# Kernel optimization log

Measured on AMD Instinct MI355X. Metric: run time of the kernel, lower is better.

The kernel has to match this reference:

```python
import jax, jax.numpy as jnp
import numpy as np

DECAY = 0.99
EPS = 1e-10
COMMIT = 0.25
K = 1024
D = 64


def setup_inputs() -> dict:
    key = jax.random.key(0)
    k1, k2, k3, k4 = jax.random.split(key, 4)
    return {
        "z_e": jax.random.normal(k1, (64, 64, 32, 32), dtype=jnp.float32),
        "embedding_w": jax.random.normal(k2, (K, D), dtype=jnp.float32),
        "ema_cluster_size": jax.random.uniform(k3, (K,), dtype=jnp.float32),
        "ema_w": jax.random.normal(k4, (K, D), dtype=jnp.float32),
    }


def reference(z_e, embedding_w, ema_cluster_size, ema_w):
    # [B, C, H, W] -> [B, H, W, C] -> [N, D]
    z_nhwc = jnp.transpose(z_e, (0, 2, 3, 1))
    z_flat = z_nhwc.reshape(-1, z_nhwc.shape[-1])

    # Squared-euclidean distances via ||z||^2 + ||e||^2 - 2 z e^T  -> [N, K]
    z_sq = jnp.sum(z_flat * z_flat, axis=1, keepdims=True)
    e_sq = jnp.sum(embedding_w * embedding_w, axis=1)
    distances = z_sq + e_sq - 2.0 * (z_flat @ embedding_w.T)

    indices = jnp.argmin(distances, axis=1)                      # [N]
    encodings = jax.nn.one_hot(indices, K, dtype=z_flat.dtype)   # [N, K]

    quantized = embedding_w[indices].reshape(z_nhwc.shape)       # [B, H, W, C]

    # --- EMA codebook update (training path; no-grad in original) ---
    counts = jnp.sum(encodings, axis=0)                          # [K]
    new_cluster_size = DECAY * ema_cluster_size + (1.0 - DECAY) * counts
    dw = encodings.T @ z_flat                                    # [K, D]
    new_ema_w = DECAY * ema_w + (1.0 - DECAY) * dw
    n = jnp.sum(new_cluster_size)
    cluster_size = (new_cluster_size + EPS) / (n + K * EPS) * n
    new_embedding_w = new_ema_w / cluster_size[:, None]

    # Commitment loss (quantized detached)
    diff = jax.lax.stop_gradient(quantized) - z_nhwc
    loss = COMMIT * jnp.mean(diff * diff)

    # Straight-through estimator
    quantized_st = z_nhwc + jax.lax.stop_gradient(quantized - z_nhwc)

    avg_probs = jnp.mean(encodings, axis=0)
    perplexity = jnp.exp(-jnp.sum(avg_probs * jnp.log(avg_probs + 1e-10)))

    quantized_out = jnp.transpose(quantized_st, (0, 3, 1, 2))    # [B, C, H, W]
    return (quantized_out, loss, perplexity, encodings,
            new_embedding_w, new_cluster_size, new_ema_w)
```

## Files before the change

### kernel.cpp

```cpp
#include <hip/hip_runtime.h>
#include <math.h>

#define NTOT 65536
#define KCB  1024
#define DIM  64

typedef float fvec2 __attribute__((ext_vector_type(2)));
typedef float fvec4 __attribute__((ext_vector_type(4)));
typedef short sh8  __attribute__((ext_vector_type(8)));

static const size_t OFF_Q    = 0;
static const size_t OFF_LOSS = 4194304;
static const size_t OFF_PERP = 4194305;
static const size_t OFF_ENC  = 4194306;
static const size_t OFF_EMB  = 71303170;
static const size_t OFF_NCS  = 71368706;
static const size_t OFF_NEMA = 71369730;

static const size_t WSO_IDX   = 0;
static const size_t WSO_ESQ   = 262144;
static const size_t WSO_LOSSP = 266240;
static const size_t WSO_CNT   = 270336;
static const size_t WSO_SCAL  = 274432;
static const size_t WSO_EBH   = 278528;
static const size_t WSO_EBL   = 409600;
static const size_t WSO_ZC    = 540672;
static const size_t WS_NEED_ZC = 540672 + (size_t)NTOT * DIM * 4;

__device__ __forceinline__ unsigned short f2bf(float f) {
    unsigned u = __builtin_bit_cast(unsigned, f);
    return (unsigned short)((u + 0x7FFFu + ((u >> 16) & 1u)) >> 16);
}
__device__ __forceinline__ float bf2f(unsigned short h) {
    unsigned u = ((unsigned)h) << 16;
    return __builtin_bit_cast(float, u);
}

__global__ void k_eprep(const float* __restrict__ emb,
                        unsigned short* __restrict__ ebh,
                        unsigned short* __restrict__ ebl,
                        float* __restrict__ esq) {
    int gid = blockIdx.x * 256 + threadIdx.x;
    int c = gid >> 3, ko8 = gid & 7;
    const fvec4* p = (const fvec4*)(emb + ((size_t)c << 6) + (ko8 << 3));
    fvec4 v0 = p[0], v1 = p[1];
    float f[8] = {v0.x, v0.y, v0.z, v0.w, v1.x, v1.y, v1.z, v1.w};
    sh8 h, l;
    float sq0 = 0.f, sq1 = 0.f;
#pragma unroll
    for (int j = 0; j < 8; ++j) {
        unsigned short hb = f2bf(f[j]);
        h[j] = (short)hb;
        l[j] = (short)f2bf(f[j] - bf2f(hb));
        if (j < 4) sq0 = fmaf(f[j], f[j], sq0); else sq1 = fmaf(f[j], f[j], sq1);
    }
    float sq = sq0 + sq1;
    sq += __shfl_xor(sq, 1, 64);
    sq += __shfl_xor(sq, 2, 64);
    sq += __shfl_xor(sq, 4, 64);
    if (ko8 == 0) esq[c] = sq;

    int ct = c >> 4, cl = c & 15, kc = ko8 >> 2, ko = ko8 & 3;
    size_t base = ((((size_t)ct << 1) + kc) << 9) + (((size_t)(ko << 4) + cl) << 3);
    *(sh8*)(ebh + base) = h;
    *(sh8*)(ebl + base) = l;
}

__global__ __launch_bounds__(256, 4)
void k_assign(const float* __restrict__ ze, const float* __restrict__ emb,
              const float* __restrict__ esq,
              const unsigned short* __restrict__ ebh,
              const unsigned short* __restrict__ ebl,
              int* __restrict__ idx_out, float* __restrict__ lossp,
              float* __restrict__ zc, int use_zc) {
    __shared__ float zt[4096];
    __shared__ float etq[4096];
    __shared__ int   sfidx[64];

    const int tid  = threadIdx.x;
    const int blk  = blockIdx.x;
    const int b    = blk >> 4;
    const int hw0  = (blk & 15) << 6;
    const int n0   = blk << 6;
    const int lane = tid & 63;
    const int wave = tid >> 6;
    const int cg   = lane & 15;
    const int ko   = lane >> 4;

#pragma unroll
    for (int j = 0; j < 4; ++j) {
        int idx = tid + (j << 8);
        int d = idx >> 4, r0 = (idx & 15) << 2;
        const fvec4 v = *(const fvec4*)(ze + (((size_t)(b << 6) + d) << 10) + hw0 + r0);
        zt[(r0 + 0) * 64 + d] = v.x;
        zt[(r0 + 1) * 64 + d] = v.y;
        zt[(r0 + 2) * 64 + d] = v.z;
        zt[(r0 + 3) * 64 + d] = v.w;
    }
    __syncthreads();

    const int arow = (wave << 4) + cg;
    sh8 Ah0, Ah1, Al0, Al1;
#pragma unroll
    for (int j = 0; j < 8; ++j) {
        float f0 = zt[arow * 64 + (ko << 3) + j];
        float f1 = zt[arow * 64 + 32 + (ko << 3) + j];
        unsigned short h0 = f2bf(f0), h1 = f2bf(f1);
        Ah0[j] = (short)h0;  Al0[j] = (short)f2bf(f0 - bf2f(h0));
        Ah1[j] = (short)h1;  Al1[j] = (short)f2bf(f1 - bf2f(h1));
    }

    float tb[4]  = {3.4e38f, 3.4e38f, 3.4e38f, 3.4e38f};
    float ts2[4] = {3.4e38f, 3.4e38f, 3.4e38f, 3.4e38f};
    int ti1[4] = {0, 0, 0, 0};
    int ti2[4] = {0, 0, 0, 0};

    const size_t lb = (size_t)lane << 3;
#define LOADB(d0, d1, d2, d3, ctv)                                  \
    { size_t o_ = ((size_t)(ctv) << 10) + lb;                       \
      d0 = *(const sh8*)(ebh + o_);                                 \
      d1 = *(const sh8*)(ebh + o_ + 512);                           \
      d2 = *(const sh8*)(ebl + o_);                                 \
      d3 = *(const sh8*)(ebl + o_ + 512); }

#define FOLD(ctv, acc)                                              \
    { const int code_ = ((ctv) << 4) + cg;                          \
      const float es_ = esq[code_];                                 \
      _Pragma("unroll")                                             \
      for (int rg = 0; rg < 4; ++rg) {                              \
          float s_ = fmaf((acc)[rg], -2.0f, es_);                   \
          bool c1 = s_ < tb[rg];                                    \
          bool c2 = s_ < ts2[rg];                                   \
          ti2[rg] = c1 ? ti1[rg] : (c2 ? code_ : ti2[rg]);          \
          ts2[rg] = c1 ? tb[rg] : (c2 ? s_ : ts2[rg]);              \
          ti1[rg] = c1 ? code_ : ti1[rg];                           \
          tb[rg]  = c1 ? s_ : tb[rg];                               \
      } }

#define TILE(i) ((((i) + (blk << 1)) & 63))

    sh8 b0h0, b0h1, b0l0, b0l1, b1h0, b1h1, b1l0, b1l1;
    LOADB(b0h0, b0h1, b0l0, b0l1, TILE(0));
    LOADB(b1h0, b1h1, b1l0, b1l1, TILE(1));

    for (int i = 0; i < 64; i += 2) {
        fvec4 aa = {0.f, 0.f, 0.f, 0.f}, ab = {0.f, 0.f, 0.f, 0.f};
        aa = __builtin_amdgcn_mfma_f32_16x16x32_bf16(Ah0, b0h0, aa, 0, 0, 0);
        ab = __builtin_amdgcn_mfma_f32_16x16x32_bf16(Ah1, b0h1, ab, 0, 0, 0);
        aa = __builtin_amdgcn_mfma_f32_16x16x32_bf16(Ah0, b0l0, aa, 0, 0, 0);
        ab = __builtin_amdgcn_mfma_f32_16x16x32_bf16(Ah1, b0l1, ab, 0, 0, 0);
        aa = __builtin_amdgcn_mfma_f32_16x16x32_bf16(Al0, b0h0, aa, 0, 0, 0);
        ab = __builtin_amdgcn_mfma_f32_16x16x32_bf16(Al1, b0h1, ab, 0, 0, 0);
        const int ct0 = TILE(i);
        if (i + 2 < 64) LOADB(b0h0, b0h1, b0l0, b0l1, TILE(i + 2));
        fvec4 acc0 = aa + ab;
        FOLD(ct0, acc0);

        fvec4 ba = {0.f, 0.f, 0.f, 0.f}, bb = {0.f, 0.f, 0.f, 0.f};
        ba = __builtin_amdgcn_mfma_f32_16x16x32_bf16(Ah0, b1h0, ba, 0, 0, 0);
        bb = __builtin_amdgcn_mfma_f32_16x16x32_bf16(Ah1, b1h1, bb, 0, 0, 0);
        ba = __builtin_amdgcn_mfma_f32_16x16x32_bf16(Ah0, b1l0, ba, 0, 0, 0);
        bb = __builtin_amdgcn_mfma_f32_16x16x32_bf16(Ah1, b1l1, bb, 0, 0, 0);
        ba = __builtin_amdgcn_mfma_f32_16x16x32_bf16(Al0, b1h0, ba, 0, 0, 0);
        bb = __builtin_amdgcn_mfma_f32_16x16x32_bf16(Al1, b1h1, bb, 0, 0, 0);
        const int ct1 = TILE(i + 1);
        if (i + 3 < 64) LOADB(b1h0, b1h1, b1l0, b1l1, TILE(i + 3));
        fvec4 acc1 = ba + bb;
        FOLD(ct1, acc1);
    }
#undef TILE
#undef LOADB
#undef FOLD

    float* mb  = etq;
    float* ms2 = etq + 1024;
    int*   mi1 = (int*)(etq + 2048);
    int*   mi2 = (int*)(etq + 3072);
#pragma unroll
    for (int rg = 0; rg < 4; ++rg) {
        int row = (wave << 4) + (ko << 2) + rg;
        mb [(cg << 6) + row] = tb[rg];
        ms2[(cg << 6) + row] = ts2[rg];
        mi1[(cg << 6) + row] = ti1[rg];
        mi2[(cg << 6) + row] = ti2[rg];
    }
    __syncthreads();

    if (tid < 64) {
        const int r = tid;
        float fb = mb[r], fs2 = ms2[r];
        int fi1 = mi1[r], fi2 = mi2[r];
#pragma unroll
        for (int p = 1; p < 16; ++p) {
            float ob = mb[(p << 6) + r], os2 = ms2[(p << 6) + r];
            int oi1 = mi1[(p << 6) + r], oi2 = mi2[(p << 6) + r];
            if (ob < fb)       { fs2 = fb; fi2 = fi1; fb = ob; fi1 = oi1; }
            else if (ob < fs2) { fs2 = ob; fi2 = oi1; }
            if (os2 < fs2)     { fs2 = os2; fi2 = oi2; }
        }
        if (fs2 - fb < 2e-2f) {
            double d1 = 0.0, d2 = 0.0;
            const float* e1 = emb + (size_t)fi1 * 64;
            const float* e2 = emb + (size_t)fi2 * 64;
            for (int d = 0; d < 64; ++d) {
                double zd = (double)zt[r * 64 + d];
                double q1 = zd - (double)e1[d];
                double q2 = zd - (double)e2[d];
                d1 += q1 * q1;
                d2 += q2 * q2;
            }
            if ((d2 < d1) || (d2 == d1 && fi2 < fi1)) fi1 = fi2;
        }
        sfidx[r] = fi1;
        idx_out[n0 + r] = fi1;
    }
    __syncthreads();

    float lacc = 0.f;
    for (int i = tid; i < 4096; i += 256) {
        int r = i >> 6, d = i & 63;
        float e  = emb[(size_t)sfidx[r] * 64 + d];
        float zv = zt[r * 64 + d];
        float df = e - zv;
        lacc = fmaf(df, df, lacc);
        if (use_zc) zc[(((size_t)(n0 + r)) << 6) + d] = zv;
    }
    __syncthreads();

    float* lred = etq;
    lred[tid] = lacc;
    __syncthreads();
    for (int s = 128; s > 0; s >>= 1) {
        if (tid < s) lred[tid] += lred[tid + s];
        __syncthreads();
    }
    if (tid == 0) lossp[blk] = lred[0];
}

__global__ __launch_bounds__(256)
void k_tail(const int* __restrict__ idx, const float* __restrict__ zcmp,
            const float* __restrict__ ze, const float* __restrict__ emaw,
            const float* __restrict__ ecs, const float* __restrict__ emb,
            float* __restrict__ out, int* __restrict__ counts, int use_zc) {
    __shared__ __align__(16) char smem[17424];
    const int t = threadIdx.x;

    if (blockIdx.x >= 1024) {
        const int blk = blockIdx.x - 1024;
        const int b   = blk >> 4;
        const int hw0 = (blk & 15) << 6;
        const int n0  = blk << 6;
        int*   sfidx = (int*)smem;
        float* qt    = (float*)(smem + 256);

        if (t < 64) sfidx[t] = idx[n0 + t];
        __syncthreads();

        for (int i = t; i < 4096; i += 256) {
            int r = i >> 6, d = i & 63;
            qt[d * 65 + r] = emb[(size_t)sfidx[r] * 64 + d];
        }

        fvec2* enc2 = (fvec2*)(out + OFF_ENC);
        for (int i = t; i < 32768; i += 256) {
            int r = i >> 9, c2 = i & 511;
            int fi = sfidx[r];
            int cb = c2 << 1;
            fvec2 v;
            v.x = (fi == cb)     ? 1.0f : 0.0f;
            v.y = (fi == cb + 1) ? 1.0f : 0.0f;
            __builtin_nontemporal_store(v, &enc2[(size_t)(n0 + r) * 512 + c2]);
        }
        __syncthreads();

        for (int i = t; i < 4096; i += 256) {
            int d = i >> 6, r = i & 63;
            __builtin_nontemporal_store(
                qt[d * 65 + r],
                &out[OFF_Q + ((size_t)((b << 6) + d) << 10) + hw0 + r]);
        }
        return;
    }

    const int k    = blockIdx.x;
    const int g    = t >> 6;
    const int d    = t & 63;
    const int lane = t & 63;
    int*   s_list = (int*)smem;
    int*   s_wsum = (int*)(smem + 16384);
    float* s_red  = (float*)(smem + 16400);

#define ZLOAD(n) (use_zc ? zcmp[((size_t)(n) << 6) + d] \
                         : ze[((((size_t)((n) >> 10) << 6) + d) << 10) + ((n) & 1023)])

    float a0 = 0.f, a1 = 0.f, a2 = 0.f, a3 = 0.f;
    int totalM = 0;

    for (int chunk = 0; chunk < 16; ++chunk) {
        const int base = chunk << 12;
        const int nb   = base + (t << 4);
        const int4* ip = (const int4*)(idx + nb);
        const int4 v0 = ip[0], v1 = ip[1], v2 = ip[2], v3 = ip[3];

        int c = 0;
        c += (v0.x == k) + (v0.y == k) + (v0.z == k) + (v0.w == k);
        c += (v1.x == k) + (v1.y == k) + (v1.z == k) + (v1.w == k);
        c += (v2.x == k) + (v2.y == k) + (v2.z == k) + (v2.w == k);
        c += (v3.x == k) + (v3.y == k) + (v3.z == k) + (v3.w == k);

        int inc = c;
#pragma unroll
        for (int off = 1; off < 64; off <<= 1) {
            int y = __shfl_up(inc, (unsigned)off, 64);
            if (lane >= off) inc += y;
        }
        if (lane == 63) s_wsum[g] = inc;
        __syncthreads();

        int wbase = 0;
#pragma unroll
        for (int w = 0; w < 4; ++w) wbase += (w < g) ? s_wsum[w] : 0;
        const int M = s_wsum[0] + s_wsum[1] + s_wsum[2] + s_wsum[3];
        int pos = wbase + inc - c;

        if (v0.x == k) s_list[pos++] = nb + 0;
        if (v0.y == k) s_list[pos++] = nb + 1;
        if (v0.z == k) s_list[pos++] = nb + 2;
        if (v0.w == k) s_list[pos++] = nb + 3;
        if (v1.x == k) s_list[pos++] = nb + 4;
        if (v1.y == k) s_list[pos++] = nb + 5;
        if (v1.z == k) s_list[pos++] = nb + 6;
        if (v1.w == k) s_list[pos++] = nb + 7;
        if (v2.x == k) s_list[pos++] = nb + 8;
        if (v2.y == k) s_list[pos++] = nb + 9;
        if (v2.z == k) s_list[pos++] = nb + 10;
        if (v2.w == k) s_list[pos++] = nb + 11;
        if (v3.x == k) s_list[pos++] = nb + 12;
        if (v3.y == k) s_list[pos++] = nb + 13;
        if (v3.z == k) s_list[pos++] = nb + 14;
        if (v3.w == k) s_list[pos++] = nb + 15;
        __syncthreads();

        int j = g;
        for (; j + 12 < M; j += 16) {
            int n0_ = s_list[j], n1_ = s_list[j + 4];
            int n2_ = s_list[j + 8], n3_ = s_list[j + 12];
            float z0 = ZLOAD(n0_), z1 = ZLOAD(n1_);
            float z2 = ZLOAD(n2_), z3 = ZLOAD(n3_);
            a0 += z0; a1 += z1; a2 += z2; a3 += z3;
        }
        for (; j < M; j += 4) a0 += ZLOAD(s_list[j]);
        totalM += M;
        __syncthreads();
    }
#undef ZLOAD

    s_red[(g << 6) + d] = (a0 + a1) + (a2 + a3);
    __syncthreads();
    if (g == 0) {
        float s = ((s_red[d] + s_red[64 + d]) + s_red[128 + d]) + s_red[192 + d];
        out[OFF_NEMA + ((size_t)k << 6) + d] =
            fmaf(0.01f, s, 0.99f * emaw[((size_t)k << 6) + d]);
    }
    if (t == 0) {
        counts[k] = totalM;
        out[OFF_NCS + k] = fmaf(0.01f, (float)totalM, 0.99f * ecs[k]);
    }
}

__global__ void k_scalars(const float* __restrict__ lossp, const int* __restrict__ counts,
                          const float* __restrict__ ncs, float* __restrict__ out,
                          float* __restrict__ scal) {
    __shared__ float sr[256];
    const int t = threadIdx.x;

    float v = lossp[t] + lossp[t + 256] + lossp[t + 512] + lossp[t + 768];
    sr[t] = v;
    __syncthreads();
    for (int s = 128; s > 0; s >>= 1) { if (t < s) sr[t] += sr[t + s]; __syncthreads(); }
    if (t == 0) out[OFF_LOSS] = sr[0] * (0.25f / 4194304.0f);
    __syncthreads();

    v = ncs[t] + ncs[t + 256] + ncs[t + 512] + ncs[t + 768];
    sr[t] = v;
    __syncthreads();
    for (int s = 128; s > 0; s >>= 1) { if (t < s) sr[t] += sr[t + s]; __syncthreads(); }
    if (t == 0) scal[0] = sr[0];
    __syncthreads();

    float pv = 0.f;
    for (int i = t; i < 1024; i += 256) {
        float p = (float)counts[i] * (1.0f / 65536.0f);
        pv += p * logf(p + 1e-10f);
    }
    sr[t] = pv;
    __syncthreads();
    for (int s = 128; s > 0; s >>= 1) { if (t < s) sr[t] += sr[t + s]; __syncthreads(); }
    if (t == 0) out[OFF_PERP] = expf(-sr[0]);
}

__global__ void k_embnorm(const float* __restrict__ nema, const float* __restrict__ ncs,
                          const float* __restrict__ scal, float* __restrict__ embw) {
    int i = blockIdx.x * 256 + threadIdx.x;
    float n = scal[0];
    int k = i >> 6;
    float cs = (ncs[k] + 1e-10f) / (n + 1.024e-7f) * n;
    embw[i] = nema[i] / cs;
}

extern "C" void kernel_launch(void* const* d_in, const int* in_sizes, int n_in,
                              void* d_out, int out_size, void* d_ws, size_t ws_size,
                              hipStream_t stream) {
    const float* ze   = (const float*)d_in[0];
    const float* emb  = (const float*)d_in[1];
    const float* ecs  = (const float*)d_in[2];
    const float* emaw = (const float*)d_in[3];
    float* out = (float*)d_out;
    char*  ws  = (char*)d_ws;

    int*            idx    = (int*)(ws + WSO_IDX);
    float*          esq    = (float*)(ws + WSO_ESQ);
    float*          lossp  = (float*)(ws + WSO_LOSSP);
    int*            counts = (int*)(ws + WSO_CNT);
    float*          scal   = (float*)(ws + WSO_SCAL);
    unsigned short* ebh    = (unsigned short*)(ws + WSO_EBH);
    unsigned short* ebl    = (unsigned short*)(ws + WSO_EBL);
    float*          zc     = (float*)(ws + WSO_ZC);
    const int use_zc = (ws_size >= WS_NEED_ZC) ? 1 : 0;

    k_eprep  <<<32,   256, 0, stream>>>(emb, ebh, ebl, esq);
    k_assign <<<1024, 256, 0, stream>>>(ze, emb, esq, ebh, ebl, idx, lossp, zc, use_zc);
    k_tail   <<<2048, 256, 0, stream>>>(idx, zc, ze, emaw, ecs, emb, out, counts, use_zc);
    k_scalars<<<1,    256, 0, stream>>>(lossp, counts, out + OFF_NCS, out, scal);
    k_embnorm<<<256,  256, 0, stream>>>(out + OFF_NEMA, out + OFF_NCS, scal, out + OFF_EMB);
}
```

Measured before the change: 184.1 us.

## Vectorize one-hot and loss stores, interleave tail block roles

The loss/zc copy loop in the argmin kernel now uses float4 loads and stores instead of scalar ones. In the tail kernel, the one-hot encoding rows are written as 16-byte float4 stores, offset by 2 floats because the encoding region starts only 8-byte aligned, with one thread handling the head and tail pairs. Odd and even block indices now alternate between the writer role and the codebook-reduction role, so both kinds of work are spread across the GPU instead of forming two separate halves. This adds index arithmetic and a thread-divergent edge case, and relies on the output offset parity for alignment.

```diff
diff --git a/kernel.cpp b/kernel.cpp
--- a/kernel.cpp
+++ b/kernel.cpp
@@ -217,13 +217,17 @@
     __syncthreads();
 
     float lacc = 0.f;
-    for (int i = tid; i < 4096; i += 256) {
-        int r = i >> 6, d = i & 63;
-        float e  = emb[(size_t)sfidx[r] * 64 + d];
-        float zv = zt[r * 64 + d];
-        float df = e - zv;
-        lacc = fmaf(df, df, lacc);
-        if (use_zc) zc[(((size_t)(n0 + r)) << 6) + d] = zv;
+    for (int i = tid; i < 1024; i += 256) {
+        int r = i >> 4, d4 = (i & 15) << 2;
+        const fvec4 zv = *(const fvec4*)&zt[(r << 6) + d4];
+        const fvec4 ev = *(const fvec4*)(emb + ((size_t)sfidx[r] << 6) + d4);
+        fvec4 df = ev - zv;
+        lacc = fmaf(df.x, df.x, lacc);
+        lacc = fmaf(df.y, df.y, lacc);
+        lacc = fmaf(df.z, df.z, lacc);
+        lacc = fmaf(df.w, df.w, lacc);
+        if (use_zc)
+            *(fvec4*)&zc[(((size_t)(n0 + r)) << 6) + d4] = zv;
     }
     __syncthreads();
 
@@ -245,8 +249,8 @@
     __shared__ __align__(16) char smem[17424];
     const int t = threadIdx.x;
 
-    if (blockIdx.x >= 1024) {
-        const int blk = blockIdx.x - 1024;
+    if (blockIdx.x & 1) {
+        const int blk = blockIdx.x >> 1;
         const int b   = blk >> 4;
         const int hw0 = (blk & 15) << 6;
         const int n0  = blk << 6;
@@ -261,15 +265,31 @@
             qt[d * 65 + r] = emb[(size_t)sfidx[r] * 64 + d];
         }
 
-        fvec2* enc2 = (fvec2*)(out + OFF_ENC);
-        for (int i = t; i < 32768; i += 256) {
-            int r = i >> 9, c2 = i & 511;
-            int fi = sfidx[r];
-            int cb = c2 << 1;
-            fvec2 v;
-            v.x = (fi == cb)     ? 1.0f : 0.0f;
-            v.y = (fi == cb + 1) ? 1.0f : 0.0f;
-            __builtin_nontemporal_store(v, &enc2[(size_t)(n0 + r) * 512 + c2]);
+        float* ebase = out + OFF_ENC;
+        if (t < 255) {
+            const int cb = 2 + (t << 2);
+            for (int r = 0; r < 64; ++r) {
+                const int fi = sfidx[r];
+                fvec4 v;
+                v.x = (fi == cb)     ? 1.0f : 0.0f;
+                v.y = (fi == cb + 1) ? 1.0f : 0.0f;
+                v.z = (fi == cb + 2) ? 1.0f : 0.0f;
+                v.w = (fi == cb + 3) ? 1.0f : 0.0f;
+                __builtin_nontemporal_store(
+                    v, (fvec4*)(ebase + ((size_t)(n0 + r) << 10) + cb));
+            }
+        } else {
+            for (int r = 0; r < 64; ++r) {
+                const int fi = sfidx[r];
+                float* rowp = ebase + ((size_t)(n0 + r) << 10);
+                fvec2 hd, tl;
+                hd.x = (fi == 0)    ? 1.0f : 0.0f;
+                hd.y = (fi == 1)    ? 1.0f : 0.0f;
+                tl.x = (fi == 1022) ? 1.0f : 0.0f;
+                tl.y = (fi == 1023) ? 1.0f : 0.0f;
+                __builtin_nontemporal_store(hd, (fvec2*)rowp);
+                __builtin_nontemporal_store(tl, (fvec2*)(rowp + 1022));
+            }
         }
         __syncthreads();
 
@@ -282,7 +302,7 @@
         return;
     }
 
-    const int k    = blockIdx.x;
+    const int k    = blockIdx.x >> 1;
     const int g    = t >> 6;
     const int d    = t & 63;
     const int lane = t & 63;
```

New measurement: 153.2 us. 16.8% less time.
